# Optimization experiments

Measured on AMD Instinct MI355X. Metric: run time of the kernel, lower is better.

## Reference

```python
import jax, jax.numpy as jnp
import numpy as np

H = 256
NUM_CONVS = 4
NUM_GRAPHS = 1024
N_PER_GRAPH = 32
ORDER = 3
NUM_TYPES = 22  # len(utils.BOND_TYPES)
NUM_NOISE_LEVEL = 50
ANNEAL_POWER = 2.0


def _build_graph():
    # Chain molecules extended to order-3 neighbors (mimics extend_graph on a path graph):
    # for |i-j| in [1,ORDER]: edge_order=|i-j|, edge_type = bond type if order 1 else NUM_TYPES+order-1.
    n = N_PER_GRAPH
    i, j = np.meshgrid(np.arange(n), np.arange(n), indexing='ij')
    dist = np.abs(i - j)
    mask = (dist >= 1) & (dist <= ORDER)
    src_l, dst_l, eo = i[mask], j[mask], dist[mask]
    offs = np.arange(NUM_GRAPHS)[:, None] * n
    src = (src_l[None, :] + offs).reshape(-1)
    dst = (dst_l[None, :] + offs).reshape(-1)
    edge_order = np.tile(eo, NUM_GRAPHS)
    rng = np.random.default_rng(0)
    bond_t = rng.integers(1, 5, size=edge_order.shape)
    edge_type = np.where(edge_order == 1, bond_t, NUM_TYPES + edge_order - 1)
    node2graph = np.repeat(np.arange(NUM_GRAPHS), n)
    return src, dst, edge_type, node2graph


def setup_inputs() -> dict:
    key = jax.random.key(0)
    ks = jax.random.split(key, 24)
    src, dst, edge_type, node2graph = _build_graph()
    N, E = node2graph.shape[0], src.shape[0]
    w = lambda k, s: (jax.random.normal(k, s, jnp.float32) * 0.05)
    sigmas = jnp.asarray(np.exp(np.linspace(np.log(10.0), np.log(0.01), NUM_NOISE_LEVEL)), dtype=jnp.float32)
    return {
        'atom_type': jnp.asarray(np.random.default_rng(1).integers(0, 100, N), jnp.int32),
        'edge_index': jnp.asarray(np.stack([src, dst]), jnp.int32),
        'edge_type': jnp.asarray(edge_type, jnp.int32),
        'node2graph': jnp.asarray(node2graph, jnp.int32),
        'noise_level': jax.random.randint(ks[0], (NUM_GRAPHS,), 0, NUM_NOISE_LEVEL, jnp.int32),
        'pos': jax.random.normal(ks[1], (N, 3), jnp.float32) * 3.0,
        'd_noise': jax.random.normal(ks[2], (E, 1), jnp.float32),
        'sigmas': sigmas,
        'node_emb': w(ks[3], (100, H)), 'edge_emb': w(ks[4], (100, H)),
        'in_W1': w(ks[5], (1, H)), 'in_b1': w(ks[6], (H,)),
        'in_W2': w(ks[7], (H, H)), 'in_b2': w(ks[8], (H,)),
        'gin_W1': w(ks[9], (NUM_CONVS, H, H)), 'gin_b1': w(ks[10], (NUM_CONVS, H)),
        'gin_W2': w(ks[11], (NUM_CONVS, H, H)), 'gin_b2': w(ks[12], (NUM_CONVS, H)),
        'out_W1': w(ks[13], (2 * H, H)), 'out_b1': w(ks[14], (H,)),
        'out_W2': w(ks[15], (H, H // 2)), 'out_b2': w(ks[16], (H // 2,)),
        'out_W3': w(ks[17], (H // 2, 1)), 'out_b3': w(ks[18], (1,)),
    }


def reference(atom_type, edge_index, edge_type, node2graph, noise_level,
              pos, d_noise, sigmas, node_emb, edge_emb,
              in_W1, in_b1, in_W2, in_b2,
              gin_W1, gin_b1, gin_W2, gin_b2,
              out_W1, out_b1, out_W2, out_b2, out_W3, out_b3):
    N = pos.shape[0]
    G = noise_level.shape[0]
    row, col = edge_index[0], edge_index[1]
    edge2graph = node2graph[row]                                  # [E]
    d = jnp.linalg.norm(pos[row] - pos[col], axis=-1, keepdims=True)  # [E,1]
    used_sigmas = sigmas[noise_level][edge2graph][:, None]        # [E,1]
    perturbed_d = d + d_noise * used_sigmas
    target = -(perturbed_d - d) / used_sigmas ** 2
    # embeddings + input MLP (Linear-relu-Linear)
    node_attr = node_emb[atom_type]                               # [N,H]
    d_emb = jax.nn.relu(perturbed_d @ in_W1 + in_b1) @ in_W2 + in_b2
    edge_attr = d_emb * edge_emb[edge_type]                       # [E,H]
    # GIN with GINE convs: agg = sum_j relu(x_j + e_ij); out = MLP(x + agg); relu between convs; residual
    x = node_attr
    n_convs = gin_W1.shape[0]
    for k in range(n_convs):
        msg = jax.nn.relu(x[row] + edge_attr)                     # [E,H]
        agg = jax.ops.segment_sum(msg, col, num_segments=N)       # [N,H]
        h = jax.nn.relu((x + agg) @ gin_W1[k] + gin_b1[k]) @ gin_W2[k] + gin_b2[k]
        if k < n_convs - 1:
            h = jax.nn.relu(h)
        x = h + x  # short_cut
    # edge score head
    feat = jnp.concatenate([x[row] * x[col], edge_attr], axis=-1)  # [E,2H]
    s = jax.nn.relu(feat @ out_W1 + out_b1)
    s = jax.nn.relu(s @ out_W2 + out_b2)
    s = s @ out_W3 + out_b3                                       # [E,1]
    scores = (s / used_sigmas).reshape(-1)
    t = target.reshape(-1)
    loss_e = 0.5 * (scores - t) ** 2 * used_sigmas.reshape(-1) ** ANNEAL_POWER
    return jax.ops.segment_sum(loss_e, edge2graph, num_segments=G)  # [G]
```

## Files before the change

### kernel.cpp

```cpp
#include <hip/hip_runtime.h>
#include <math.h>

typedef unsigned int u32;
typedef __attribute__((ext_vector_type(8))) short bf16x8;
typedef __attribute__((ext_vector_type(4))) float f32x4;

#define MFMA16(a,b,c) __builtin_amdgcn_mfma_f32_16x16x32_bf16(a,b,c,0,0,0)

__device__ inline u32 bf16r(float x){
  u32 u = __float_as_uint(x);
  return (u + 0x7fffu + ((u >> 16) & 1u)) >> 16;
}
__device__ inline u32 pack2(float a, float b){ return bf16r(a) | (bf16r(b) << 16); }
__device__ inline uint4 pack8(const float* f){
  uint4 v; v.x = pack2(f[0],f[1]); v.y = pack2(f[2],f[3]);
  v.z = pack2(f[4],f[5]); v.w = pack2(f[6],f[7]); return v;
}
__device__ inline float bf2f(short s){ return __uint_as_float(((u32)(unsigned short)s) << 16); }

__device__ __forceinline__ void gload_lds16(const void* g, void* l){
  __builtin_amdgcn_global_load_lds((const __attribute__((address_space(1))) unsigned int*)g,
                                   (__attribute__((address_space(3))) unsigned int*)l,
                                   16, 0, 0);
}

__device__ __forceinline__ int frag_off(int f, int quad){
  return (f>>1)*64 + (f&1)*32 + ((quad ^ ((f>>1)&3))*8);
}

__device__ __forceinline__ int xg(int g, int r){ return g ^ ((r ^ (g>>3)) & 7); }

__global__ void k_cvtAll(const float* __restrict__ inW2, const float* __restrict__ gW1,
                         const float* __restrict__ gW2, const float* __restrict__ oW1,
                         const float* __restrict__ oW2,
                         short* __restrict__ w2t, short* __restrict__ gw1t,
                         short* __restrict__ gw2t, short* __restrict__ ow1t,
                         short* __restrict__ ow2t){
  int gidx = blockIdx.x*256 + threadIdx.x;
  const float* src; short* dst; int t, K8, Nf;
  if (gidx < 8192)      { src = inW2; dst = w2t; t = gidx; K8 = 32; Nf = 256; }
  else if (gidx < 40960){ int r = gidx-8192;  int c = r>>13; t = r&8191;
                          src = gW1 + (size_t)c*65536; dst = gw1t + (size_t)c*65536; K8 = 32; Nf = 256; }
  else if (gidx < 73728){ int r = gidx-40960; int c = r>>13; t = r&8191;
                          src = gW2 + (size_t)c*65536; dst = gw2t + (size_t)c*65536; K8 = 32; Nf = 256; }
  else if (gidx < 90112){ t = gidx-73728; src = oW1; dst = ow1t; K8 = 64; Nf = 256; }
  else if (gidx < 94208){ t = gidx-90112; src = oW2; dst = ow2t; K8 = 32; Nf = 128; }
  else return;
  int f = t / K8, c = t - f*K8;
  float v[8];
  #pragma unroll
  for (int j=0;j<8;j++) v[j] = src[(size_t)(c*8+j)*Nf + f];
  ((uint4*)dst)[t] = pack8(v);
}

__global__ void k_pre(const int* __restrict__ ei, const int* __restrict__ n2g,
                      const int* __restrict__ nl, const float* __restrict__ sigmas,
                      const float* __restrict__ pos, const float* __restrict__ dn, int E,
                      float* __restrict__ pd, int* __restrict__ cnt, int* __restrict__ inlist){
  int e = blockIdx.x*256 + threadIdx.x;
  if (e >= E) return;
  int r = ei[e], c = ei[E+e];
  float sg = sigmas[nl[n2g[r]]];
  float dx = pos[3*r]-pos[3*c], dy = pos[3*r+1]-pos[3*c+1], dz = pos[3*r+2]-pos[3*c+2];
  float d = sqrtf(dx*dx + dy*dy + dz*dz);
  pd[e] = d + dn[e]*sg;
  int slot = atomicAdd(&cnt[c], 1);
  if (slot < 8) inlist[c*8 + slot] = e;
}

__global__ __launch_bounds__(256) void k_attr(
    const float* __restrict__ pd, const float* __restrict__ W1, const float* __restrict__ b1,
    const short* __restrict__ W2t, const float* __restrict__ b2,
    const int* __restrict__ etype, const float* __restrict__ eemb,
    short* __restrict__ attr, int E)
{
  int tid = threadIdx.x;
  int base = blockIdx.x*64;
  int wv = tid>>6, lane = tid&63, quad = lane>>4, l15 = lane&15;
  float pdv[4];
  #pragma unroll
  for (int nt=0;nt<4;nt++) pdv[nt] = pd[base + nt*16 + l15];
  f32x4 acc[4][4];
  #pragma unroll
  for (int mt=0;mt<4;mt++) for (int nt=0;nt<4;nt++) acc[mt][nt] = (f32x4)0.f;
  #pragma unroll
  for (int s=0; s<8; s++){
    int k0 = s*32 + quad*8;
    float4 w1a = *(const float4*)(W1 + k0), w1b = *(const float4*)(W1 + k0 + 4);
    float4 b1a = *(const float4*)(b1 + k0), b1b = *(const float4*)(b1 + k0 + 4);
    bf16x8 a[4], b[4];
    #pragma unroll
    for (int mt=0;mt<4;mt++){
      int f = (wv*4+mt)*16 + l15;
      a[mt] = *(const bf16x8*)(W2t + (size_t)f*256 + k0);
    }
    #pragma unroll
    for (int nt=0;nt<4;nt++){
      float p = pdv[nt];
      float f[8] = {fmaxf(p*w1a.x+b1a.x,0.f), fmaxf(p*w1a.y+b1a.y,0.f),
                    fmaxf(p*w1a.z+b1a.z,0.f), fmaxf(p*w1a.w+b1a.w,0.f),
                    fmaxf(p*w1b.x+b1b.x,0.f), fmaxf(p*w1b.y+b1b.y,0.f),
                    fmaxf(p*w1b.z+b1b.z,0.f), fmaxf(p*w1b.w+b1b.w,0.f)};
      uint4 u = pack8(f);
      b[nt] = *(bf16x8*)&u;
    }
    #pragma unroll
    for (int mt=0;mt<4;mt++)
      #pragma unroll
      for (int nt=0;nt<4;nt++)
        acc[mt][nt] = MFMA16(a[mt], b[nt], acc[mt][nt]);
  }
  #pragma unroll
  for (int nt=0;nt<4;nt++){
    int e = base + nt*16 + l15;
    int et = etype[e];
    #pragma unroll
    for (int mt=0;mt<4;mt++){
      int f0 = (wv*4+mt)*16 + quad*4;
      float4 bb = *(const float4*)(b2 + f0);
      float4 em = *(const float4*)(eemb + (size_t)et*256 + f0);
      float v0 = (acc[mt][nt][0]+bb.x)*em.x, v1 = (acc[mt][nt][1]+bb.y)*em.y;
      float v2 = (acc[mt][nt][2]+bb.z)*em.z, v3 = (acc[mt][nt][3]+bb.w)*em.w;
      uint2 v; v.x = pack2(v0,v1); v.y = pack2(v2,v3);
      *(uint2*)(attr + (size_t)e*256 + f0) = v;
    }
  }
}

#define EPG 180
__global__ __launch_bounds__(512,1) void k_conv4(
    const int* __restrict__ at, const float* __restrict__ nemb,
    const short* __restrict__ attrS, const int* __restrict__ ei,
    const int* __restrict__ cnt, const int* __restrict__ inlist,
    const short* __restrict__ gw1t, const float* __restrict__ gb1,
    const short* __restrict__ gw2t, const float* __restrict__ gb2,
    short* __restrict__ xF)
{
  __shared__ float xls[32*256];
  __shared__ uint4 AlsV[32*32];
  __shared__ uint4 T1V [32*32];
  __shared__ uint4 attrLV[EPG*32];
  short* Als = (short*)AlsV;
  short* T1  = (short*)T1V;
  short* attrL = (short*)AlsV;
  attrL = (short*)attrLV;
  int tid = threadIdx.x;
  int nbase = blockIdx.x*32;
  int ebase = blockIdx.x*EPG;
  int wv = tid>>6, lane = tid&63, quad = lane>>4, l15 = lane&15;
  int jl = tid>>4, ch = tid&15;
  {
    const char* src = (const char*)(attrS + (size_t)ebase*256) + lane*16;
    char* dst = (char*)attrLV;
    #pragma unroll
    for (int i=0; i<12; i++){
      int r = i*8 + wv;
      if (r < 90) gload_lds16(src + r*1024, dst + r*1024);
    }
  }
  int deg;
  int eid[8], rl[8];
  {
    int j = nbase + jl;
    deg = min(cnt[j], 8);
    #pragma unroll
    for (int s=0;s<8;s++){
      int e = (s < deg) ? inlist[j*8 + s] : ebase;
      eid[s] = e - ebase;
      rl[s]  = (s < deg) ? (ei[e] - nbase) : 0;
    }
  }
  {
    int a = at[nbase + jl];
    const float4* src = (const float4*)nemb + (size_t)a*64 + ch*4;
    float* xrow = xls + jl*256;
    #pragma unroll
    for (int q=0;q<4;q++)
      *(float4*)(xrow + (xg(ch*4+q, jl)<<2)) = src[q];
  }
  __syncthreads();
  for (int c=0; c<4; c++){
    const short* W1t = gw1t + (size_t)c*65536;
    const short* W2t = gw2t + (size_t)c*65536;
    const float* b1 = gb1 + c*256;
    const float* b2 = gb2 + c*256;
    {
      float f[16];
      const float* xrow = xls + jl*256;
      #pragma unroll
      for (int q=0;q<4;q++){
        float4 v = *(const float4*)(xrow + (xg(ch*4+q, jl)<<2));
        f[q*4]=v.x; f[q*4+1]=v.y; f[q*4+2]=v.z; f[q*4+3]=v.w;
      }
      #pragma unroll
      for (int s=0; s<8; s++){
        if (s < deg){
          int r = rl[s];
          const float* xr = xls + r*256;
          const short* ar = attrL + eid[s]*256 + ch*16;
          #pragma unroll
          for (int q=0;q<4;q++){
            float4 xv = *(const float4*)(xr + (xg(ch*4+q, r)<<2));
            uint2 a2 = *(const uint2*)(ar + q*4);
            f[q*4]   += fmaxf(xv.x + __uint_as_float(a2.x<<16), 0.f);
            f[q*4+1] += fmaxf(xv.y + __uint_as_float(a2.x&0xffff0000u), 0.f);
            f[q*4+2] += fmaxf(xv.z + __uint_as_float(a2.y<<16), 0.f);
            f[q*4+3] += fmaxf(xv.w + __uint_as_float(a2.y&0xffff0000u), 0.f);
          }
        }
      }
      #pragma unroll
      for (int qq=0;qq<2;qq++){
        int cc = ch*2 + qq;
        *(uint4*)(Als + jl*256 + ((cc ^ (jl&7))*8)) = pack8(f + qq*8);
      }
    }
    __syncthreads();
    f32x4 acc[2][2];
    #pragma unroll
    for (int mt=0;mt<2;mt++) for (int nt=0;nt<2;nt++) acc[mt][nt] = (f32x4)0.f;
    #pragma unroll
    for (int s=0; s<8; s++){
      bf16x8 a[2], b[2];
      #pragma unroll
      for (int mt=0;mt<2;mt++)
        a[mt] = *(const bf16x8*)(W1t + (size_t)((wv*2+mt)*16 + l15)*256 + s*32 + quad*8);
      #pragma unroll
      for (int nt=0;nt<2;nt++){
        int n = nt*16 + l15; int cc = s*4 + quad;
        b[nt] = *(const bf16x8*)(Als + n*256 + ((cc ^ (n&7))*8));
      }
      #pragma unroll
      for (int mt=0;mt<2;mt++)
        #pragma unroll
        for (int nt=0;nt<2;nt++)
          acc[mt][nt] = MFMA16(a[mt], b[nt], acc[mt][nt]);
    }
    #pragma unroll
    for (int mt=0;mt<2;mt++){
      int f0 = (wv*2+mt)*16 + quad*4;
      float4 bb = *(const float4*)(b1 + f0);
      int cg = f0 >> 3, off = (quad&1)*4;
      #pragma unroll
      for (int nt=0;nt<2;nt++){
        int n = nt*16 + l15;
        float v0 = fmaxf(acc[mt][nt][0]+bb.x,0.f), v1 = fmaxf(acc[mt][nt][1]+bb.y,0.f);
        float v2 = fmaxf(acc[mt][nt][2]+bb.z,0.f), v3 = fmaxf(acc[mt][nt][3]+bb.w,0.f);
        uint2 v; v.x = pack2(v0,v1); v.y = pack2(v2,v3);
        *(uint2*)(T1 + n*256 + ((cg ^ (n&7))*8) + off) = v;
      }
    }
    __syncthreads();
    f32x4 acc2[2][2];
    #pragma unroll
    for (int mt=0;mt<2;mt++) for (int nt=0;nt<2;nt++) acc2[mt][nt] = (f32x4)0.f;
    #pragma unroll
    for (int s=0; s<8; s++){
      bf16x8 a[2], b[2];
      #pragma unroll
      for (int mt=0;mt<2;mt++)
        a[mt] = *(const bf16x8*)(W2t + (size_t)((wv*2+mt)*16 + l15)*256 + s*32 + quad*8);
      #pragma unroll
      for (int nt=0;nt<2;nt++){
        int n = nt*16 + l15; int cc = s*4 + quad;
        b[nt] = *(const bf16x8*)(T1 + n*256 + ((cc ^ (n&7))*8));
      }
      #pragma unroll
      for (int mt=0;mt<2;mt++)
        #pragma unroll
        for (int nt=0;nt<2;nt++)
          acc2[mt][nt] = MFMA16(a[mt], b[nt], acc2[mt][nt]);
    }
    #pragma unroll
    for (int mt=0;mt<2;mt++){
      int f0 = (wv*2+mt)*16 + quad*4;
      float4 bb = *(const float4*)(b2 + f0);
      int g = f0 >> 2;
      #pragma unroll
      for (int nt=0;nt<2;nt++){
        int n = nt*16 + l15;
        float* px = xls + n*256 + (xg(g, n)<<2);
        float4 xv = *(float4*)px;
        float h0 = acc2[mt][nt][0]+bb.x, h1 = acc2[mt][nt][1]+bb.y;
        float h2 = acc2[mt][nt][2]+bb.z, h3 = acc2[mt][nt][3]+bb.w;
        if (c < 3){ h0=fmaxf(h0,0.f); h1=fmaxf(h1,0.f); h2=fmaxf(h2,0.f); h3=fmaxf(h3,0.f); }
        xv.x += h0; xv.y += h1; xv.z += h2; xv.w += h3;
        *(float4*)px = xv;
      }
    }
    __syncthreads();
  }
  {
    const float* xrow = xls + jl*256;
    float f[16];
    #pragma unroll
    for (int q=0;q<4;q++){
      float4 v = *(const float4*)(xrow + (xg(ch*4+q, jl)<<2));
      f[q*4]=v.x; f[q*4+1]=v.y; f[q*4+2]=v.z; f[q*4+3]=v.w;
    }
    #pragma unroll
    for (int qq=0;qq<2;qq++)
      *(uint4*)(xF + (size_t)(nbase+jl)*256 + ch*16 + qq*8) = pack8(f + qq*8);
  }
}

__global__ __launch_bounds__(256,2) void k_head(
    const short* __restrict__ xF, const short* __restrict__ attrS,
    const int* __restrict__ ei,
    const short* __restrict__ W1t, const float* __restrict__ ob1,
    const short* __restrict__ W2t, const float* __restrict__ ob2,
    const float* __restrict__ W3, const float* __restrict__ ob3,
    const float* __restrict__ dnoise, const int* __restrict__ n2g,
    float* __restrict__ out, int E, int G)
{
  __shared__ uint4 BlsV[16*256];
  __shared__ float Sedge[64];
  __shared__ float part[4];
  short* Bls = (short*)BlsV;
  short* T   = (short*)BlsV;
  int tid = threadIdx.x;
  int base = blockIdx.x*64;
  int wv = tid>>6, lane = tid&63, quad = lane>>4, l15 = lane&15;
  if (tid < 64) Sedge[tid] = 0.f;
  if (tid < 4) part[tid] = 0.f;
  {
    int g = wv*64 + lane;
    int p = g>>3, hi = (g>>2)&1, cs = g&3;
    int n = p*2 + hi, cc = cs ^ (p&3);
    const short* srcb = attrS + (size_t)(base+n)*256 + cc*8;
    #pragma unroll
    for (int s=8; s<16; s++)
      gload_lds16(srcb + (s-8)*32, (char*)Bls + (size_t)s*4096 + wv*1024);
  }
  {
    int g = tid;
    int p = g>>3, hi = (g>>2)&1, cs = g&3;
    int n = p*2 + hi, cc = cs ^ (p&3);
    int rr = ei[base+n], rc = ei[E+base+n];
    const short* xr = xF + (size_t)rr*256 + cc*8;
    const short* xc = xF + (size_t)rc*256 + cc*8;
    #pragma unroll
    for (int s=0; s<8; s++){
      bf16x8 va = *(const bf16x8*)(xr + s*32);
      bf16x8 vb = *(const bf16x8*)(xc + s*32);
      float f[8];
      #pragma unroll
      for (int j=0;j<8;j++) f[j] = bf2f(va[j])*bf2f(vb[j]);
      *(uint4*)(Bls + (size_t)s*2048 + g*8) = pack8(f);
    }
  }
  __syncthreads();
  f32x4 acc[4][4];
  #pragma unroll
  for (int mt=0;mt<4;mt++) for (int nt=0;nt<4;nt++) acc[mt][nt] = (f32x4)0.f;
  #pragma unroll
  for (int s=0; s<16; s++){
    bf16x8 a[4], b[4];
    #pragma unroll
    for (int mt=0;mt<4;mt++)
      a[mt] = *(const bf16x8*)(W1t + (size_t)((wv*4+mt)*16 + l15)*512 + s*32 + quad*8);
    #pragma unroll
    for (int nt=0;nt<4;nt++)
      b[nt] = *(const bf16x8*)(Bls + (size_t)s*2048 + frag_off(nt*16 + l15, quad));
    #pragma unroll
    for (int mt=0;mt<4;mt++)
      #pragma unroll
      for (int nt=0;nt<4;nt++)
        acc[mt][nt] = MFMA16(a[mt], b[nt], acc[mt][nt]);
  }
  __syncthreads();
  #pragma unroll
  for (int mt=0;mt<4;mt++){
    int f0 = (wv*4+mt)*16 + quad*4;
    float4 bb = *(const float4*)(ob1 + f0);
    int c = f0 >> 3, off = (quad&1)*4;
    #pragma unroll
    for (int nt=0;nt<4;nt++){
      int n = nt*16 + l15;
      float v0 = fmaxf(acc[mt][nt][0]+bb.x,0.f), v1 = fmaxf(acc[mt][nt][1]+bb.y,0.f);
      float v2 = fmaxf(acc[mt][nt][2]+bb.z,0.f), v3 = fmaxf(acc[mt][nt][3]+bb.w,0.f);
      uint2 v; v.x = pack2(v0,v1); v.y = pack2(v2,v3);
      *(uint2*)(T + n*256 + ((c ^ (n&7))*8) + off) = v;
    }
  }
  __syncthreads();
  f32x4 acc2[2][4];
  #pragma unroll
  for (int mt=0;mt<2;mt++) for (int nt=0;nt<4;nt++) acc2[mt][nt] = (f32x4)0.f;
  #pragma unroll
  for (int s=0; s<8; s++){
    bf16x8 a[2], b[4];
    #pragma unroll
    for (int mt=0;mt<2;mt++)
      a[mt] = *(const bf16x8*)(W2t + (size_t)((wv*2+mt)*16 + l15)*256 + s*32 + quad*8);
    #pragma unroll
    for (int nt=0;nt<4;nt++){
      int n = nt*16 + l15; int cc = s*4 + quad;
      b[nt] = *(const bf16x8*)(T + n*256 + ((cc ^ (n&7))*8));
    }
    #pragma unroll
    for (int mt=0;mt<2;mt++)
      #pragma unroll
      for (int nt=0;nt<4;nt++)
        acc2[mt][nt] = MFMA16(a[mt], b[nt], acc2[mt][nt]);
  }
  float4 b2v[2], w3v[2];
  #pragma unroll
  for (int mt=0;mt<2;mt++){
    int f0 = (wv*2+mt)*16 + quad*4;
    b2v[mt] = *(const float4*)(ob2 + f0);
    w3v[mt] = *(const float4*)(W3 + f0);
  }
  #pragma unroll
  for (int nt=0;nt<4;nt++){
    float p = 0.f;
    #pragma unroll
    for (int mt=0;mt<2;mt++){
      p += fmaxf(acc2[mt][nt][0]+b2v[mt].x,0.f)*w3v[mt].x;
      p += fmaxf(acc2[mt][nt][1]+b2v[mt].y,0.f)*w3v[mt].y;
      p += fmaxf(acc2[mt][nt][2]+b2v[mt].z,0.f)*w3v[mt].z;
      p += fmaxf(acc2[mt][nt][3]+b2v[mt].w,0.f)*w3v[mt].w;
    }
    p += __shfl_xor(p, 16);
    p += __shfl_xor(p, 32);
    if (lane < 16) atomicAdd(&Sedge[nt*16 + l15], p);
  }
  __syncthreads();
  int gbase = n2g[ei[base]];
  if (tid < 64){
    int e = base + tid;
    float sv = Sedge[tid] + ob3[0] + dnoise[e];
    float l = 0.5f*sv*sv;
    int g = n2g[ei[e]] - gbase;
    atomicAdd(&part[g & 3], l);
  }
  __syncthreads();
  if (tid < 2 && (gbase + tid) < G)
    atomicAdd(&out[gbase + tid], part[tid]);
}

static inline size_t alignup(size_t v){ return (v + 255) & ~(size_t)255; }

extern "C" void kernel_launch(void* const* d_in, const int* in_sizes, int n_in,
                              void* d_out, int out_size, void* d_ws, size_t ws_size,
                              hipStream_t stream) {
  const int*   at    = (const int*)  d_in[0];
  const int*   ei    = (const int*)  d_in[1];
  const int*   etype = (const int*)  d_in[2];
  const int*   n2g   = (const int*)  d_in[3];
  const int*   nl    = (const int*)  d_in[4];
  const float* pos   = (const float*)d_in[5];
  const float* dnoi  = (const float*)d_in[6];
  const float* sig   = (const float*)d_in[7];
  const float* nemb  = (const float*)d_in[8];
  const float* eemb  = (const float*)d_in[9];
  const float* inW1  = (const float*)d_in[10];
  const float* inb1  = (const float*)d_in[11];
  const float* inW2  = (const float*)d_in[12];
  const float* inb2  = (const float*)d_in[13];
  const float* gW1   = (const float*)d_in[14];
  const float* gb1   = (const float*)d_in[15];
  const float* gW2   = (const float*)d_in[16];
  const float* gb2   = (const float*)d_in[17];
  const float* oW1   = (const float*)d_in[18];
  const float* ob1   = (const float*)d_in[19];
  const float* oW2   = (const float*)d_in[20];
  const float* ob2   = (const float*)d_in[21];
  const float* oW3   = (const float*)d_in[22];
  const float* ob3   = (const float*)d_in[23];
  float* out = (float*)d_out;

  const int N = in_sizes[0];
  const int E = in_sizes[2];
  const int G = in_sizes[4];
  const int H = 256;

  char* w = (char*)d_ws;
  size_t off = 0;
  size_t o_attr  = off; off = alignup(off + (size_t)E*H*2);
  size_t o_xF    = off; off = alignup(off + (size_t)N*H*2);
  size_t o_pd    = off; off = alignup(off + (size_t)E*4);
  size_t o_cnt   = off; off = alignup(off + (size_t)N*4);
  size_t o_inl   = off; off = alignup(off + (size_t)N*8*4);
  size_t o_w2t   = off; off = alignup(off + (size_t)H*H*2);
  size_t o_gw1t  = off; off = alignup(off + (size_t)4*H*H*2);
  size_t o_gw2t  = off; off = alignup(off + (size_t)4*H*H*2);
  size_t o_ow1t  = off; off = alignup(off + (size_t)H*2*H*2);
  size_t o_ow2t  = off; off = alignup(off + (size_t)(H/2)*H*2);
  (void)ws_size; (void)n_in; (void)out_size;

  short* attrS = (short*)(w + o_attr);
  short* xF    = (short*)(w + o_xF);
  float* pd    = (float*)(w + o_pd);
  int*   cnt   = (int*)  (w + o_cnt);
  int*   inl   = (int*)  (w + o_inl);
  short* w2t   = (short*)(w + o_w2t);
  short* gw1t  = (short*)(w + o_gw1t);
  short* gw2t  = (short*)(w + o_gw2t);
  short* ow1t  = (short*)(w + o_ow1t);
  short* ow2t  = (short*)(w + o_ow2t);

  hipMemsetAsync(cnt, 0, (size_t)N*4, stream);
  hipMemsetAsync(out, 0, (size_t)G*4, stream);

  k_cvtAll<<<368, 256, 0, stream>>>(inW2, gW1, gW2, oW1, oW2,
                                    w2t, gw1t, gw2t, ow1t, ow2t);

  k_pre<<<(E+255)/256, 256, 0, stream>>>(ei, n2g, nl, sig, pos, dnoi, E, pd, cnt, inl);
  k_attr<<<E/64, 256, 0, stream>>>(pd, inW1, inb1, w2t, inb2, etype, eemb, attrS, E);

  k_conv4<<<G, 512, 0, stream>>>(at, nemb, attrS, ei, cnt, inl,
                                 gw1t, gb1, gw2t, gb2, xF);

  k_head<<<E/64, 256, 0, stream>>>(xF, attrS, ei, ow1t, ob1, ow2t, ob2,
                                   oW3, ob3, dnoi, n2g, out, E, G);
}
```

Baseline: 531.5 us.

## Drop LDS staging of edge attributes, read from global, allow two blocks per CU

Removes the per-block LDS buffer that prefetched each graph's 180 edge-attribute rows with global_load_lds. The aggregation loop now reads edge attributes straight from global memory with 16-byte vector loads, inside every conv iteration. Freeing the large LDS allocation and raising launch bounds to two blocks per CU is meant to increase occupancy and hide latency. In exchange, the attributes are re-read from global or cache in each of the four convs, and the tighter register budget may cause spills.

Result: faster. 507.0 us (-4.6%).

```diff
diff --git a/kernel.cpp b/kernel.cpp
--- a/kernel.cpp
+++ b/kernel.cpp
@@ -127,8 +127,7 @@
   }
 }
 
-#define EPG 180
-__global__ __launch_bounds__(512,1) void k_conv4(
+__global__ __launch_bounds__(512,2) void k_conv4(
     const int* __restrict__ at, const float* __restrict__ nemb,
     const short* __restrict__ attrS, const int* __restrict__ ei,
     const int* __restrict__ cnt, const int* __restrict__ inlist,
@@ -139,25 +138,12 @@
   __shared__ float xls[32*256];
   __shared__ uint4 AlsV[32*32];
   __shared__ uint4 T1V [32*32];
-  __shared__ uint4 attrLV[EPG*32];
   short* Als = (short*)AlsV;
   short* T1  = (short*)T1V;
-  short* attrL = (short*)AlsV;
-  attrL = (short*)attrLV;
   int tid = threadIdx.x;
   int nbase = blockIdx.x*32;
-  int ebase = blockIdx.x*EPG;
   int wv = tid>>6, lane = tid&63, quad = lane>>4, l15 = lane&15;
   int jl = tid>>4, ch = tid&15;
-  {
-    const char* src = (const char*)(attrS + (size_t)ebase*256) + lane*16;
-    char* dst = (char*)attrLV;
-    #pragma unroll
-    for (int i=0; i<12; i++){
-      int r = i*8 + wv;
-      if (r < 90) gload_lds16(src + r*1024, dst + r*1024);
-    }
-  }
   int deg;
   int eid[8], rl[8];
   {
@@ -165,8 +151,8 @@
     deg = min(cnt[j], 8);
     #pragma unroll
     for (int s=0;s<8;s++){
-      int e = (s < deg) ? inlist[j*8 + s] : ebase;
-      eid[s] = e - ebase;
+      int e = (s < deg) ? inlist[j*8 + s] : 0;
+      eid[s] = e;
       rl[s]  = (s < deg) ? (ei[e] - nbase) : 0;
     }
   }
@@ -197,15 +183,18 @@
         if (s < deg){
           int r = rl[s];
           const float* xr = xls + r*256;
-          const short* ar = attrL + eid[s]*256 + ch*16;
+          const short* ar = attrS + (size_t)eid[s]*256 + ch*16;
+          uint4 a4a = *(const uint4*)(ar);
+          uint4 a4b = *(const uint4*)(ar + 8);
+          u32 us[8] = {a4a.x,a4a.y,a4a.z,a4a.w, a4b.x,a4b.y,a4b.z,a4b.w};
           #pragma unroll
           for (int q=0;q<4;q++){
             float4 xv = *(const float4*)(xr + (xg(ch*4+q, r)<<2));
-            uint2 a2 = *(const uint2*)(ar + q*4);
-            f[q*4]   += fmaxf(xv.x + __uint_as_float(a2.x<<16), 0.f);
-            f[q*4+1] += fmaxf(xv.y + __uint_as_float(a2.x&0xffff0000u), 0.f);
-            f[q*4+2] += fmaxf(xv.z + __uint_as_float(a2.y<<16), 0.f);
-            f[q*4+3] += fmaxf(xv.w + __uint_as_float(a2.y&0xffff0000u), 0.f);
+            u32 lo = us[2*q], hi = us[2*q+1];
+            f[q*4]   += fmaxf(xv.x + __uint_as_float(lo<<16), 0.f);
+            f[q*4+1] += fmaxf(xv.y + __uint_as_float(lo&0xffff0000u), 0.f);
+            f[q*4+2] += fmaxf(xv.z + __uint_as_float(hi<<16), 0.f);
+            f[q*4+3] += fmaxf(xv.w + __uint_as_float(hi&0xffff0000u), 0.f);
           }
         }
       }
```
